# Optimization experiments

Hardware: AMD Instinct MI355X
Metric: run time of the kernel (lower is better)

The kernel has to match this reference:

```python
import jax, jax.numpy as jnp
import numpy as np

NUM_QUBITS = 512
NUM_CORES = 16
CORE_SIZE = 64
HIDDEN = 128
BATCH = 2048


def setup_inputs() -> dict:
    key = jax.random.key(0)
    k1, k2, k3 = jax.random.split(key, 3)
    last_assignment = jax.random.randint(k1, (BATCH, NUM_QUBITS), 0, NUM_CORES, dtype=jnp.int32)
    adjacency = jnp.ones((NUM_CORES, NUM_CORES), dtype=jnp.float32)  # all-to-all core graph
    qubit_embedding = jax.random.normal(k2, (NUM_QUBITS + 1, HIDDEN), dtype=jnp.float32)
    gcn_weight = jax.random.normal(k3, (HIDDEN, HIDDEN), dtype=jnp.float32) * (1.0 / np.sqrt(HIDDEN))
    gcn_bias = jnp.zeros((HIDDEN,), dtype=jnp.float32)
    return {
        'last_assignment': last_assignment,
        'adjacency': adjacency,
        'qubit_embedding': qubit_embedding,
        'gcn_weight': gcn_weight,
        'gcn_bias': gcn_bias,
    }


def reference(last_assignment, adjacency, qubit_embedding, gcn_weight, gcn_bias):
    B, Q = last_assignment.shape
    C = adjacency.shape[0]
    # --- replace the sequential per-qubit scatter loop with a single cumsum ---
    # pos[b,q] = number of earlier qubits assigned to the same core (the loop's
    # running counter idx); core index C (the extra row) always writes slot 0
    # because the loop resets its counter every iteration.
    oh = jax.nn.one_hot(last_assignment, C + 1, dtype=jnp.int32)        # [B,Q,C+1]
    cnt = jnp.cumsum(oh, axis=1)                                        # inclusive counts
    pos = jnp.take_along_axis(cnt, last_assignment[..., None], axis=2)[..., 0] - 1
    pos = jnp.where(last_assignment == C, 0, pos)
    buf = jnp.full((B, C + 1, CORE_SIZE), Q, dtype=jnp.int32)           # padding id = num_qubits
    b_idx = jnp.arange(B)[:, None]
    q_idx = jnp.broadcast_to(jnp.arange(Q, dtype=jnp.int32)[None, :], (B, Q))
    buf = buf.at[b_idx, last_assignment, pos].set(q_idx, mode='drop')
    buf = buf[:, :C, :]                                                 # drop overflow core row
    # --- embedding (padding row forced to zero, as nn.Embedding padding_idx) ---
    tbl = qubit_embedding.at[Q].set(0.0)
    qubit_embs = tbl[buf]                                               # [B,C,core_size,H]
    core_embs = qubit_embs.max(axis=2)                                  # [B,C,H]
    # --- GCNConv(add_self_loops=False): D^{-1/2} A D^{-1/2} (X W^T) + b ---
    deg = adjacency.sum(axis=0)
    dinv = jnp.where(deg > 0, 1.0 / jnp.sqrt(deg), 0.0)
    a_norm = adjacency * dinv[:, None] * dinv[None, :]                  # symmetric norm
    h = jnp.einsum('bch,oh->bco', core_embs, gcn_weight)                # lin (PyG: x @ W^T)
    out = jnp.einsum('ij,bjo->bio', a_norm, h) + gcn_bias               # [B,C,H]
    return out
```

## Files before the change

kernel.cpp:

```cpp
#include <hip/hip_runtime.h>
#include <stdint.h>

typedef unsigned short u16;
typedef unsigned int u32;
typedef unsigned long long u64;

typedef __bf16 bf16x8 __attribute__((ext_vector_type(8)));
typedef float f32x4 __attribute__((ext_vector_type(4)));
typedef u16 u16x8 __attribute__((ext_vector_type(8)));

#define NQ 512
#define NC 16
#define NH 128
#define NB 2048
#define QE_KEYS (513*128)
#define WT_OFF  QE_KEYS
#define GW_ELEMS (128*128)
#define A_OFF (WT_OFF + GW_ELEMS)
#define LSEG 1088
#define ESEG 2304
#define ESTRIDE 136

static __device__ __forceinline__ u16 f2bf_rne(float f){
  u32 u = __float_as_uint(f);
  u += 0x7fffu + ((u>>16)&1u);
  return (u16)(u>>16);
}
static __device__ __forceinline__ u32 pack_rne(float lo, float hi){
  return (u32)f2bf_rne(lo) | ((u32)f2bf_rne(hi)<<16);
}
static __device__ __forceinline__ u16 key_of(float f){
  u16 b = f2bf_rne(f);
  return (b & 0x8000u) ? (u16)~b : (u16)(b | 0x8000u);
}
static __device__ __forceinline__ u16 unkey(u16 k){
  return (k & 0x8000u) ? (u16)(k ^ 0x8000u) : (u16)~k;
}

union Frag { u32 u[4]; uint4 u4; bf16x8 f; };
union U8   { u16x8 v; int w[4]; uint4 u4; u16 h[8]; };

__global__ void prepass_kernel(const float* __restrict__ qe,
                               const float* __restrict__ gw,
                               const float* __restrict__ adj,
                               u16* __restrict__ ws)
{
  if (blockIdx.x == 0) {
    __shared__ float sD[16];
    int t = threadIdx.x;
    if (t < 16) {
      float s = 0.f;
      for (int i = 0; i < 16; ++i) s += adj[i*16 + t];
      sD[t] = (s > 0.f) ? (1.0f / sqrtf(s)) : 0.f;
    }
    __syncthreads();
    int i = t >> 4, jp = (t & 15) * 2;
    float lo = (jp   < 16) ? adj[i*16 + jp]   * sD[i] * sD[jp]   : 0.f;
    float hi = (jp+1 < 16) ? adj[i*16 + jp+1] * sD[i] * sD[jp+1] : 0.f;
    ((u32*)(ws + A_OFF))[t] = pack_rne(lo, hi);
    return;
  }
  int idx = (blockIdx.x - 1) * 256 + threadIdx.x;
  if (idx < QE_KEYS/8) {
    int i8 = idx * 8;
    uint4 o;
    if (i8 >= 512*NH) {
      o.x = 0x80008000u; o.y = 0x80008000u; o.z = 0x80008000u; o.w = 0x80008000u;
    } else {
      const float4* p = (const float4*)(qe + i8);
      float4 a = p[0], b = p[1];
      o.x = (u32)key_of(a.x) | ((u32)key_of(a.y)<<16);
      o.y = (u32)key_of(a.z) | ((u32)key_of(a.w)<<16);
      o.z = (u32)key_of(b.x) | ((u32)key_of(b.y)<<16);
      o.w = (u32)key_of(b.z) | ((u32)key_of(b.w)<<16);
    }
    *(uint4*)(ws + i8) = o;
  } else if (idx < QE_KEYS/8 + GW_ELEMS/8) {
    int j8 = (idx - QE_KEYS/8) * 8;
    const float4* p = (const float4*)(gw + j8);
    float4 a = p[0], b = p[1];
    uint4 o;
    o.x = pack_rne(a.x, a.y); o.y = pack_rne(a.z, a.w);
    o.z = pack_rne(b.x, b.y); o.w = pack_rne(b.z, b.w);
    *(uint4*)(ws + WT_OFF + j8) = o;
  }
}

static __device__ __forceinline__ void wave_reduce_max(U8& A){
  U8 B;
  #pragma unroll
  for (int j = 0; j < 4; ++j) B.w[j] = __shfl_xor(A.w[j], 16);
  A.v = __builtin_elementwise_max(A.v, B.v);
  #pragma unroll
  for (int j = 0; j < 4; ++j) B.w[j] = __shfl_xor(A.w[j], 32);
  A.v = __builtin_elementwise_max(A.v, B.v);
}

__global__ __launch_bounds__(256, 4)
void core_snapshot_kernel(const int* __restrict__ la,
                          const u16* __restrict__ ws,
                          const float* __restrict__ gb,
                          float* __restrict__ outp)
{
  __shared__ __align__(16) u16 sListAll[2*LSEG];
  __shared__ __align__(16) u16 sEAll[2*ESEG];
  __shared__ int sCnt[2][2][16];

  const int tid  = threadIdx.x;
  const int lane = tid & 63;
  const int wv   = tid >> 6;
  const int it   = wv >> 1;
  const int tw   = wv & 1;
  const int m    = lane & 15;
  const int quad = lane >> 4;
  const int item = blockIdx.x*2 + it;
  u16* sList = sListAll + it*LSEG;
  u16* sE    = sEAll    + it*ESEG;
  const u16* qt = ws;
  const u16* wt = ws + WT_OFF;

  {
    uint4 f = make_uint4(0x02000200u,0x02000200u,0x02000200u,0x02000200u);
    *(uint4*)&sList[tw*512 + lane*8] = f;
  }
  __syncthreads();

  int av[4];
  #pragma unroll
  for (int ch = 0; ch < 4; ++ch) av[ch] = la[item*NQ + (tw*4 + ch)*64 + lane];
  const u64 lmask = (1ull << lane) - 1ull;
  u32 runbase = 0;
  u32 rankrel[4];
  #pragma unroll
  for (int ch = 0; ch < 4; ++ch) {
    u32 cnt = 0, intra = 0;
    #pragma unroll
    for (int c = 0; c < 16; ++c) {
      u64 mk = __ballot(av[ch] == c);
      if (lane == c)    cnt   = (u32)__popcll(mk);
      if (av[ch] == c)  intra = (u32)__popcll(mk & lmask);
    }
    u32 base = (u32)__shfl((int)runbase, av[ch]);
    rankrel[ch] = base + intra;
    runbase += cnt;
  }
  if (lane < 16) sCnt[it][tw][lane] = (int)runbase;
  if (tw == 0) {
    #pragma unroll
    for (int ch = 0; ch < 4; ++ch) {
      u32 rank = rankrel[ch];
      if (rank < 64) sList[av[ch]*64 + (rank&3)*16 + (rank>>2)] = (u16)(ch*64 + lane);
    }
  }
  __syncthreads();
  u32 cntv;
  if (tw == 1) {
    #pragma unroll
    for (int ch = 0; ch < 4; ++ch) {
      u32 rank = (u32)sCnt[it][0][av[ch]] + rankrel[ch];
      if (rank < 64) sList[av[ch]*64 + (rank&3)*16 + (rank>>2)] = (u16)((4 + ch)*64 + lane);
    }
    cntv = runbase + (u32)((lane < 16) ? sCnt[it][0][lane] : 0);
  } else {
    cntv = runbase + (u32)((lane < 16) ? sCnt[it][1][lane] : 0);
  }
  __syncthreads();

  const u16* qb = qt + m*8;
  for (int cc = 0; cc < 8; ++cc) {
    int c = tw*8 + cc;
    int cnt = __shfl((int)cntv, c);
    U8 S0, S1;
    S0.u4 = *(const uint4*)&sList[c*64 + quad*16];
    S1.u4 = *(const uint4*)&sList[c*64 + quad*16 + 8];
    U8 A; A.v = (u16x8)0;
    {
      U8 T[8];
      #pragma unroll
      for (int k = 0; k < 8; ++k) T[k].u4 = *(const uint4*)(qb + (int)S0.h[k]*NH);
      #pragma unroll
      for (int k = 0; k < 8; ++k) A.v = __builtin_elementwise_max(A.v, T[k].v);
    }
    if (cnt > 32) {
      U8 T[4];
      #pragma unroll
      for (int k = 0; k < 4; ++k) T[k].u4 = *(const uint4*)(qb + (int)S1.h[k]*NH);
      #pragma unroll
      for (int k = 0; k < 4; ++k) A.v = __builtin_elementwise_max(A.v, T[k].v);
    }
    if (cnt > 48) {
      U8 T[4];
      #pragma unroll
      for (int k = 0; k < 4; ++k) T[k].u4 = *(const uint4*)(qb + (int)S1.h[4+k]*NH);
      #pragma unroll
      for (int k = 0; k < 4; ++k) A.v = __builtin_elementwise_max(A.v, T[k].v);
    }
    wave_reduce_max(A);
    if (cnt < 64) {
      U8 Z; Z.v = (u16x8)(u16)0x8000u;
      A.v = __builtin_elementwise_max(A.v, Z.v);
    }
    if (quad == 0) {
      uint4 e;
      e.x = (u32)unkey(A.h[0]) | ((u32)unkey(A.h[1])<<16);
      e.y = (u32)unkey(A.h[2]) | ((u32)unkey(A.h[3])<<16);
      e.z = (u32)unkey(A.h[4]) | ((u32)unkey(A.h[5])<<16);
      e.w = (u32)unkey(A.h[6]) | ((u32)unkey(A.h[7])<<16);
      *(uint4*)&sE[c*ESTRIDE + m*8] = e;
    }
  }
  __syncthreads();

  bf16x8 af[4];
  #pragma unroll
  for (int ks = 0; ks < 4; ++ks)
    af[ks] = *(const bf16x8*)&sE[m*ESTRIDE + ks*32 + quad*8];
  Frag anf;
  anf.u4 = *(const uint4*)(ws + A_OFF + m*32 + quad*8);

  #pragma unroll
  for (int tt = 0; tt < 4; ++tt) {
    int t = tw*4 + tt;
    f32x4 acc = {0.f, 0.f, 0.f, 0.f};
    #pragma unroll
    for (int ks = 0; ks < 4; ++ks) {
      bf16x8 bfr = *(const bf16x8*)(wt + (t*16 + m)*NH + ks*32 + quad*8);
      acc = __builtin_amdgcn_mfma_f32_16x16x32_bf16(af[ks], bfr, acc, 0, 0, 0);
    }
    float d16[4], d32[4], lo[4], hi[4];
    #pragma unroll
    for (int r = 0; r < 4; ++r) {
      d16[r] = __shfl_down(acc[r], 16);
      d32[r] = __shfl_down(acc[r], 32);
    }
    #pragma unroll
    for (int r = 0; r < 4; ++r) {
      lo[r] = (quad == 0) ? acc[r] : d16[r];
      hi[r] = (quad == 0) ? d16[r] : d32[r];
    }
    Frag hb;
    hb.u[0] = pack_rne(lo[0], lo[1]); hb.u[1] = pack_rne(lo[2], lo[3]);
    hb.u[2] = pack_rne(hi[0], hi[1]); hb.u[3] = pack_rne(hi[2], hi[3]);
    if (quad >= 2) { hb.u[0]=0; hb.u[1]=0; hb.u[2]=0; hb.u[3]=0; }
    float biasv = gb[t*16 + m];
    f32x4 o4 = {biasv, biasv, biasv, biasv};
    o4 = __builtin_amdgcn_mfma_f32_16x16x32_bf16(anf.f, hb.f, o4, 0, 0, 0);
    float* op = outp + item*(NC*NH) + t*16 + m;
    #pragma unroll
    for (int r = 0; r < 4; ++r) op[(quad*4 + r)*NH] = o4[r];
  }
}

extern "C" void kernel_launch(void* const* d_in, const int* in_sizes, int n_in,
                              void* d_out, int out_size, void* d_ws, size_t ws_size,
                              hipStream_t stream) {
  const int*   la  = (const int*)d_in[0];
  const float* adj = (const float*)d_in[1];
  const float* qe  = (const float*)d_in[2];
  const float* gw  = (const float*)d_in[3];
  const float* gb  = (const float*)d_in[4];
  float* outp = (float*)d_out;
  u16* ws = (u16*)d_ws;

  int pre_blocks = 1 + (QE_KEYS/8 + GW_ELEMS/8 + 255)/256;
  prepass_kernel<<<pre_blocks, 256, 0, stream>>>(qe, gw, adj, ws);
  core_snapshot_kernel<<<NB/2, 256, 0, stream>>>(la, ws, gb, outp);
}
```

Measured before the change: 90.45 us.

## Process core pairs per iteration and defer cross-quad max reduction to LDS

The gather loop now handles two cores per iteration and issues both cores' first eight embedding loads before reducing either, so more memory requests are in flight per wave. The wave-level shuffle max reduction is removed: each quad writes its partial max to a separate LDS slab. The fragment-load stage then reads the four partials, reduces them, and un-keys two halves at a time with a branchless word-level routine. This trades shuffles and serialised latency for a fourfold larger sE buffer, which may reduce occupancy, and higher register pressure from holding two sets of loads.

After: 89.05 us (median of 2 runs). No clear change (-1.5%).

```diff
diff --git a/kernel.cpp b/kernel.cpp
--- a/kernel.cpp
+++ b/kernel.cpp
@@ -18,8 +18,8 @@
 #define GW_ELEMS (128*128)
 #define A_OFF (WT_OFF + GW_ELEMS)
 #define LSEG 1088
-#define ESEG 2304
-#define ESTRIDE 136
+#define ESTC 544
+#define ESEG (16*ESTC)
 
 static __device__ __forceinline__ u16 f2bf_rne(float f){
   u32 u = __float_as_uint(f);
@@ -33,12 +33,13 @@
   u16 b = f2bf_rne(f);
   return (b & 0x8000u) ? (u16)~b : (u16)(b | 0x8000u);
 }
-static __device__ __forceinline__ u16 unkey(u16 k){
-  return (k & 0x8000u) ? (u16)(k ^ 0x8000u) : (u16)~k;
+static __device__ __forceinline__ u32 unkey2(u32 w){
+  u32 s = w & 0x80008000u;
+  return w ^ ~(s - (s >> 15));
 }
 
 union Frag { u32 u[4]; uint4 u4; bf16x8 f; };
-union U8   { u16x8 v; int w[4]; uint4 u4; u16 h[8]; };
+union U8   { u16x8 v; int w[4]; u32 uw[4]; uint4 u4; u16 h[8]; };
 
 __global__ void prepass_kernel(const float* __restrict__ qe,
                                const float* __restrict__ gw,
@@ -86,16 +87,6 @@
   }
 }
 
-static __device__ __forceinline__ void wave_reduce_max(U8& A){
-  U8 B;
-  #pragma unroll
-  for (int j = 0; j < 4; ++j) B.w[j] = __shfl_xor(A.w[j], 16);
-  A.v = __builtin_elementwise_max(A.v, B.v);
-  #pragma unroll
-  for (int j = 0; j < 4; ++j) B.w[j] = __shfl_xor(A.w[j], 32);
-  A.v = __builtin_elementwise_max(A.v, B.v);
-}
-
 __global__ __launch_bounds__(256, 4)
 void core_snapshot_kernel(const int* __restrict__ la,
                           const u16* __restrict__ ws,
@@ -167,54 +158,81 @@
   __syncthreads();
 
   const u16* qb = qt + m*8;
-  for (int cc = 0; cc < 8; ++cc) {
-    int c = tw*8 + cc;
-    int cnt = __shfl((int)cntv, c);
-    U8 S0, S1;
-    S0.u4 = *(const uint4*)&sList[c*64 + quad*16];
-    S1.u4 = *(const uint4*)&sList[c*64 + quad*16 + 8];
+  #pragma unroll 1
+  for (int pp = 0; pp < 4; ++pp) {
+    const int c0 = tw*8 + pp*2, c1 = c0 + 1;
+    const int cnt0 = __shfl((int)cntv, c0);
+    const int cnt1 = __shfl((int)cntv, c1);
+    U8 S0a, S1a, S0b, S1b;
+    S0a.u4 = *(const uint4*)&sList[c0*64 + quad*16];
+    S1a.u4 = *(const uint4*)&sList[c0*64 + quad*16 + 8];
+    S0b.u4 = *(const uint4*)&sList[c1*64 + quad*16];
+    S1b.u4 = *(const uint4*)&sList[c1*64 + quad*16 + 8];
+    U8 Ta[8], Tb[8];
+    #pragma unroll
+    for (int k = 0; k < 8; ++k) Ta[k].u4 = *(const uint4*)(qb + (int)S0a.h[k]*NH);
+    #pragma unroll
+    for (int k = 0; k < 8; ++k) Tb[k].u4 = *(const uint4*)(qb + (int)S0b.h[k]*NH);
+
     U8 A; A.v = (u16x8)0;
-    {
-      U8 T[8];
-      #pragma unroll
-      for (int k = 0; k < 8; ++k) T[k].u4 = *(const uint4*)(qb + (int)S0.h[k]*NH);
-      #pragma unroll
-      for (int k = 0; k < 8; ++k) A.v = __builtin_elementwise_max(A.v, T[k].v);
-    }
-    if (cnt > 32) {
-      U8 T[4];
-      #pragma unroll
-      for (int k = 0; k < 4; ++k) T[k].u4 = *(const uint4*)(qb + (int)S1.h[k]*NH);
+    #pragma unroll
+    for (int k = 0; k < 8; ++k) A.v = __builtin_elementwise_max(A.v, Ta[k].v);
+    if (cnt0 > 32) {
+      U8 T[4];
+      #pragma unroll
+      for (int k = 0; k < 4; ++k) T[k].u4 = *(const uint4*)(qb + (int)S1a.h[k]*NH);
       #pragma unroll
       for (int k = 0; k < 4; ++k) A.v = __builtin_elementwise_max(A.v, T[k].v);
     }
-    if (cnt > 48) {
-      U8 T[4];
-      #pragma unroll
-      for (int k = 0; k < 4; ++k) T[k].u4 = *(const uint4*)(qb + (int)S1.h[4+k]*NH);
+    if (cnt0 > 48) {
+      U8 T[4];
+      #pragma unroll
+      for (int k = 0; k < 4; ++k) T[k].u4 = *(const uint4*)(qb + (int)S1a.h[4+k]*NH);
       #pragma unroll
       for (int k = 0; k < 4; ++k) A.v = __builtin_elementwise_max(A.v, T[k].v);
     }
-    wave_reduce_max(A);
-    if (cnt < 64) {
-      U8 Z; Z.v = (u16x8)(u16)0x8000u;
-      A.v = __builtin_elementwise_max(A.v, Z.v);
-    }
-    if (quad == 0) {
-      uint4 e;
-      e.x = (u32)unkey(A.h[0]) | ((u32)unkey(A.h[1])<<16);
-      e.y = (u32)unkey(A.h[2]) | ((u32)unkey(A.h[3])<<16);
-      e.z = (u32)unkey(A.h[4]) | ((u32)unkey(A.h[5])<<16);
-      e.w = (u32)unkey(A.h[6]) | ((u32)unkey(A.h[7])<<16);
-      *(uint4*)&sE[c*ESTRIDE + m*8] = e;
-    }
+    if (cnt0 < 64) { U8 Z; Z.v = (u16x8)(u16)0x8000u; A.v = __builtin_elementwise_max(A.v, Z.v); }
+    *(uint4*)&sE[c0*ESTC + quad*136 + m*8] = A.u4;
+
+    U8 B; B.v = (u16x8)0;
+    #pragma unroll
+    for (int k = 0; k < 8; ++k) B.v = __builtin_elementwise_max(B.v, Tb[k].v);
+    if (cnt1 > 32) {
+      U8 T[4];
+      #pragma unroll
+      for (int k = 0; k < 4; ++k) T[k].u4 = *(const uint4*)(qb + (int)S1b.h[k]*NH);
+      #pragma unroll
+      for (int k = 0; k < 4; ++k) B.v = __builtin_elementwise_max(B.v, T[k].v);
+    }
+    if (cnt1 > 48) {
+      U8 T[4];
+      #pragma unroll
+      for (int k = 0; k < 4; ++k) T[k].u4 = *(const uint4*)(qb + (int)S1b.h[4+k]*NH);
+      #pragma unroll
+      for (int k = 0; k < 4; ++k) B.v = __builtin_elementwise_max(B.v, T[k].v);
+    }
+    if (cnt1 < 64) { U8 Z; Z.v = (u16x8)(u16)0x8000u; B.v = __builtin_elementwise_max(B.v, Z.v); }
+    *(uint4*)&sE[c1*ESTC + quad*136 + m*8] = B.u4;
   }
   __syncthreads();
 
   bf16x8 af[4];
   #pragma unroll
-  for (int ks = 0; ks < 4; ++ks)
-    af[ks] = *(const bf16x8*)&sE[m*ESTRIDE + ks*32 + quad*8];
+  for (int ks = 0; ks < 4; ++ks) {
+    const u16* pb = &sE[m*ESTC + ks*32 + quad*8];
+    U8 P0, P1, P2, P3;
+    P0.u4 = *(const uint4*)(pb);
+    P1.u4 = *(const uint4*)(pb + 136);
+    P2.u4 = *(const uint4*)(pb + 272);
+    P3.u4 = *(const uint4*)(pb + 408);
+    P0.v = __builtin_elementwise_max(P0.v, P1.v);
+    P2.v = __builtin_elementwise_max(P2.v, P3.v);
+    P0.v = __builtin_elementwise_max(P0.v, P2.v);
+    Frag f;
+    #pragma unroll
+    for (int j = 0; j < 4; ++j) f.u[j] = unkey2(P0.uw[j]);
+    af[ks] = f.f;
+  }
   Frag anf;
   anf.u4 = *(const uint4*)(ws + A_OFF + m*32 + quad*8);
 
```
